# Kernel optimization log

Measured on AMD Instinct MI355X. Metric: run time of the kernel, lower is better.

## Reference

```python
import jax, jax.numpy as jnp
import numpy as np
from jax import lax

B, C, H, W = 4, 64, 256, 256
T, Q = 16, 0.2
C2 = 2 * C


def conv2d(x, w, b, pad):
    y = lax.conv_general_dilated(x, w, (1, 1), [(pad, pad), (pad, pad)],
                                 dimension_numbers=('NCHW', 'OIHW', 'NCHW'))
    return y + b[None, :, None, None]


def setup_inputs() -> dict:
    key = jax.random.key(0)
    ks = jax.random.split(key, 10)
    x = jax.random.normal(ks[0], (B, C, H, W), dtype=jnp.float32)
    lms = jax.random.normal(ks[1], (B, 4, H, W), dtype=jnp.float32)
    # params (kaiming-ish scale)
    W_conv = jax.random.normal(ks[2], (C2, C, 3, 3), dtype=jnp.float32) * (1.0 / np.sqrt(C * 9))
    b_conv = jnp.zeros((C2,), dtype=jnp.float32)
    W_out = jax.random.normal(ks[3], (4, C2), dtype=jnp.float32) * (1.0 / np.sqrt(C2))  # 1x1 conv as matrix
    b_out = jnp.zeros((4,), dtype=jnp.float32)
    W_aue = jax.random.normal(ks[4], (4, C2, 3, 3), dtype=jnp.float32) * (1.0 / np.sqrt(C2 * 9))
    b_aue = jnp.zeros((4,), dtype=jnp.float32)
    # T Bernoulli(1-q) channel masks, fixed for reproducibility  [T, 2C]
    masks = jax.random.bernoulli(ks[5], 1.0 - Q, (T, C2)).astype(jnp.float32)
    return {"x": x, "lms": lms, "W_conv": W_conv, "b_conv": b_conv,
            "W_out": W_out, "b_out": b_out, "W_aue": W_aue, "b_aue": b_aue,
            "masks": masks}


def reference(x, lms, W_conv, b_conv, W_out, b_out, W_aue, b_aue, masks):
    # feature extraction: 3x3 conv C -> 2C
    h = conv2d(x, W_conv, b_conv, 1)                      # [B, 2C, H, W]
    # MC-dropout samples: out(mask_t * h) == (W_out * mask_t) @ h  (1x1 conv is linear)
    Wt = W_out[None, :, :] * masks[:, None, :]            # [T, 4, 2C]
    samples = jnp.tanh(jnp.einsum('toc,bchw->tbohw', Wt, h)
                       + b_out[None, None, :, None, None]) + lms[None]  # [T, B, 4, H, W]
    mean = jnp.mean(samples, axis=0)
    EU = jnp.var(samples, axis=0, ddof=1)                 # unbiased variance over T
    AU = jax.nn.sigmoid(conv2d(h, W_aue, b_aue, 1))       # [B, 4, H, W]
    return (AU, EU, mean)
```

## Files before the change

### kernel.cpp

```cpp
#include <hip/hip_runtime.h>

#define Bsz 4
#define Cin 64
#define C2c 128
#define Hh 256
#define Ww 256
#define Tt 16
#define HW (Hh*Ww)
#define PLANE (Bsz*4*HW)

typedef __attribute__((ext_vector_type(8))) short bf16x8;
typedef __attribute__((ext_vector_type(4))) float f32x4;

#define XT_OFF  0
#define WBF_OFF 33554432
#define WTB_OFF 33701888
#define AUB_OFF 33718272
#define ZP_OFF  33727488

#define N_WTB 8192
#define N_WBF 73728
#define N_AUB 4608
#define N_ZP  64

__device__ __forceinline__ unsigned short f2bf(float f) {
  union { float f; unsigned u; } cv; cv.f = f;
  unsigned u = cv.u;
  unsigned r = (u + 0x7fffu + ((u >> 16) & 1u)) >> 16;
  return (unsigned short)r;
}

__device__ __forceinline__ unsigned cvtpk(float a, float b) {
  unsigned r;
  asm("v_cvt_pk_bf16_f32 %0, %1, %2" : "=v"(r) : "v"(a), "v"(b));
  return r;
}

union U8 { uint2 u2[2]; uint4 u4; bf16x8 v; };

#define GLOAD16(g, l) __builtin_amdgcn_global_load_lds( \
    (const __attribute__((address_space(1))) unsigned int*)(g), \
    (__attribute__((address_space(3))) unsigned int*)(l), 16, 0, 0)

__global__ __launch_bounds__(256) void xtp_kernel(
    const float* __restrict__ x, const float* __restrict__ W_out,
    const float* __restrict__ masks, const float* __restrict__ Wc,
    const float* __restrict__ W_aue,
    unsigned short* __restrict__ xT, unsigned short* __restrict__ Wtb,
    unsigned short* __restrict__ Wbf, unsigned short* __restrict__ Aub,
    unsigned short* __restrict__ Zp) {
  __shared__ unsigned short xs[64 * 132];
  const int tid = threadIdx.x;

  if (blockIdx.z == 4) {
    int i = (blockIdx.y * 2 + blockIdx.x) * 256 + tid;
    if (i < N_WTB) {
      int to = i >> 7, c = i & 127;
      int t = to >> 2, o = to & 3;
      Wtb[i] = f2bf(W_out[o * C2c + c] * masks[t * C2c + c]);
    } else if (i < N_WTB + N_WBF) {
      int idx = i - N_WTB;
      int j = idx & 7;
      int lane = (idx >> 3) & 63;
      int nt = (idx >> 9) & 7;
      int c = idx >> 12;
      int qq = lane >> 4;
      int tap = c >> 1;
      int ic = (c & 1) * 32 + qq * 8 + j;
      int n = nt * 16 + (lane & 15);
      Wbf[idx] = f2bf(Wc[((size_t)n * Cin + ic) * 9 + tap]);
    } else if (i < N_WTB + N_WBF + N_AUB) {
      int idx = i - N_WTB - N_WBF;
      int m = idx / 1152, k = idx % 1152;
      int tap = k >> 7, c = k & 127;
      Aub[idx] = f2bf(W_aue[((size_t)m * C2c + c) * 9 + tap]);
    } else if (i < N_WTB + N_WBF + N_AUB + N_ZP) {
      Zp[i - N_WTB - N_WBF - N_AUB] = 0;
    }
    return;
  }

  const int x0 = blockIdx.x * 128, y = blockIdx.y, bi = blockIdx.z;
  #pragma unroll
  for (int i = 0; i < 8; ++i) {
    int idx = i * 256 + tid;
    int ic = idx >> 5, xq = idx & 31;
    float4 v = *(const float4*)(x + (((size_t)bi * Cin + ic) * Hh + y) * Ww + x0 + xq * 4);
    *(uint2*)(&xs[ic * 132 + xq * 4]) = make_uint2(cvtpk(v.x, v.y), cvtpk(v.z, v.w));
  }
  __syncthreads();
  #pragma unroll
  for (int j = 0; j < 4; ++j) {
    int idx = j * 256 + tid;
    int px = idx >> 3, icg = idx & 7;
    unsigned short u[8];
    #pragma unroll
    for (int k = 0; k < 8; ++k) u[k] = xs[(icg * 8 + k) * 132 + px];
    *(uint4*)(xT + (((size_t)bi * Hh + y) * Ww + (x0 + px)) * Cin + icg * 8) = *(uint4*)u;
  }
}

__global__ __launch_bounds__(256, 3) void fused_kernel(
    const unsigned short* __restrict__ xT, const unsigned short* __restrict__ Wbf,
    const unsigned short* __restrict__ Wtb, const unsigned short* __restrict__ Aub,
    const unsigned short* __restrict__ Zp,
    const float* __restrict__ bc, const float* __restrict__ b_out,
    const float* __restrict__ b_aue, const float* __restrict__ lms,
    float* __restrict__ out) {
  __shared__ __align__(16) unsigned short sh[23040];
  const int tid = threadIdx.x;
  const int x0 = blockIdx.x * 16, y0 = blockIdx.y * 8, bi = blockIdx.z;

  #pragma unroll
  for (int hf = 0; hf < 2; ++hf) {
    #pragma unroll
    for (int i = 0; i < 4; ++i) {
      int g = i * 256 + tid;
      int r = g >> 2;
      int l = (g & 3) ^ (r & 3);
      int pr = r / 20, pc = r - pr * 20;
      int gy = y0 - 2 + pr, gx = x0 - 2 + pc;
      bool ok = (r < 240) && ((unsigned)gy < Hh) && ((unsigned)gx < Ww);
      const unsigned short* src = ok
        ? xT + (((size_t)bi * Hh + gy) * Ww + gx) * Cin + (hf * 4 + l) * 8
        : Zp;
      GLOAD16(src, &sh[hf * 8192 + g * 8]);
    }
  }

  const int lane = tid & 63, wv = tid >> 6;
  const int n16 = lane & 15, q = lane >> 4;

  int rbase[3];
  #pragma unroll
  for (int s = 0; s < 3; ++s) {
    int px = (wv * 3 + s) * 16 + n16;
    int pr = px / 18, pc = px % 18;
    rbase[s] = pr * 20 + pc;
  }

  f32x4 acc[3][8];
  #pragma unroll
  for (int s = 0; s < 3; ++s)
    #pragma unroll
    for (int mt = 0; mt < 8; ++mt) acc[s][mt] = (f32x4){0.f, 0.f, 0.f, 0.f};

  asm volatile("s_waitcnt vmcnt(4)" ::: "memory");
  __builtin_amdgcn_s_barrier();
  __builtin_amdgcn_sched_barrier(0);

  #pragma unroll
  for (int hf = 0; hf < 2; ++hf) {
    if (hf == 1) {
      asm volatile("s_waitcnt vmcnt(0)" ::: "memory");
      __builtin_amdgcn_s_barrier();
      __builtin_amdgcn_sched_barrier(0);
    }
    #pragma unroll
    for (int tap = 0; tap < 9; ++tap) {
      const int dd = (tap / 3) * 20 + (tap % 3);
      const int c = tap * 2 + hf;
      bf16x8 xfr[3];
      #pragma unroll
      for (int s = 0; s < 3; ++s) {
        int rr = rbase[s] + dd;
        int a = hf * 8192 + rr * 32 + ((q ^ (rr & 3)) << 3);
        U8 t; t.u4 = *(const uint4*)(&sh[a]);
        xfr[s] = t.v;
      }
      #pragma unroll
      for (int mh = 0; mh < 2; ++mh) {
        bf16x8 wfr[4];
        const unsigned short* wb = Wbf + ((size_t)(c * 8 + mh * 4) * 64 + lane) * 8;
        #pragma unroll
        for (int i4 = 0; i4 < 4; ++i4)
          wfr[i4] = ((const U8*)(wb + i4 * 512))->v;
        __builtin_amdgcn_s_setprio(1);
        #pragma unroll
        for (int s = 0; s < 3; ++s)
          #pragma unroll
          for (int i4 = 0; i4 < 4; ++i4)
            acc[s][mh * 4 + i4] =
              __builtin_amdgcn_mfma_f32_16x16x32_bf16(wfr[i4], xfr[s], acc[s][mh * 4 + i4], 0, 0, 0);
        __builtin_amdgcn_s_setprio(0);
      }
    }
  }
  __syncthreads();

  #pragma unroll
  for (int s = 0; s < 3; ++s) {
    const int px = (wv * 3 + s) * 16 + n16;
    if (px < 180) {
      const int pr = px / 18, pc = px % 18;
      const int gy = y0 - 1 + pr, gx = x0 - 1 + pc;
      const bool valid = ((unsigned)gy < Hh) && ((unsigned)gx < Ww);
      const int key = px & 15;
      #pragma unroll
      for (int mt = 0; mt < 8; ++mt) {
        const int oc0 = mt * 16 + q * 4;
        const float4 b4 = *(const float4*)(bc + oc0);
        unsigned lo = cvtpk(acc[s][mt][0] + b4.x, acc[s][mt][1] + b4.y);
        unsigned hi = cvtpk(acc[s][mt][2] + b4.z, acc[s][mt][3] + b4.w);
        if (!valid) { lo = 0u; hi = 0u; }
        int a = px * 128 + (((mt * 2 + (q >> 1)) ^ key) << 3) + (q & 1) * 4;
        *(uint2*)(&sh[a]) = make_uint2(lo, hi);
      }
    }
  }
  __syncthreads();

  f32x4 accG[2][4];
  f32x4 accA[2];
  #pragma unroll
  for (int nt = 0; nt < 2; ++nt) {
    accA[nt] = (f32x4){0.f, 0.f, 0.f, 0.f};
    #pragma unroll
    for (int mt = 0; mt < 4; ++mt) accG[nt][mt] = (f32x4){0.f, 0.f, 0.f, 0.f};
  }

  #pragma unroll
  for (int kc = 0; kc < 4; ++kc) {
    bf16x8 afr[4];
    #pragma unroll
    for (int mt = 0; mt < 4; ++mt)
      afr[mt] = ((const U8*)(Wtb + (size_t)(mt * 16 + n16) * C2c + kc * 32 + q * 8))->v;
    #pragma unroll
    for (int nt = 0; nt < 2; ++nt) {
      int hr = (wv * 2 + nt + 1) * 18 + n16 + 1;
      int a = hr * 128 + (((kc * 4 + q) ^ (hr & 15)) << 3);
      U8 b; b.u4 = *(const uint4*)(&sh[a]);
      #pragma unroll
      for (int mt = 0; mt < 4; ++mt)
        accG[nt][mt] = __builtin_amdgcn_mfma_f32_16x16x32_bf16(afr[mt], b.v, accG[nt][mt], 0, 0, 0);
    }
  }

  #pragma unroll
  for (int kc = 0; kc < 36; ++kc) {
    const int tap = kc >> 2, co4 = kc & 3;
    const int dy = tap / 3, dx = tap % 3;
    bf16x8 afr = ((const U8*)(Aub + (size_t)(n16 & 3) * 1152 + kc * 32 + q * 8))->v;
    #pragma unroll
    for (int nt = 0; nt < 2; ++nt) {
      int hr = (wv * 2 + nt + dy) * 18 + n16 + dx;
      int a = hr * 128 + (((co4 * 4 + q) ^ (hr & 15)) << 3);
      U8 b; b.u4 = *(const uint4*)(&sh[a]);
      accA[nt] = __builtin_amdgcn_mfma_f32_16x16x32_bf16(afr, b.v, accA[nt], 0, 0, 0);
    }
  }

  const float b0 = b_out[0], b1 = b_out[1], b2 = b_out[2], b3 = b_out[3];
  const float ba = b_aue[q];
  const int px = x0 + n16;
  #pragma unroll
  for (int nt = 0; nt < 2; ++nt) {
    const int y = y0 + wv * 2 + nt;
    float th[4][4];
    #pragma unroll
    for (int mt = 0; mt < 4; ++mt) {
      #pragma unroll
      for (int r = 0; r < 4; ++r) {
        float bo = (r == 0) ? b0 : (r == 1) ? b1 : (r == 2) ? b2 : b3;
        float v = accG[nt][mt][r] + bo;
        float e = __expf(2.f * v);
        th[mt][r] = 1.f - 2.f / (e + 1.f);
      }
    }
    float mean_r[4], eu_r[4];
    #pragma unroll
    for (int r = 0; r < 4; ++r) {
      float s = th[0][r] + th[1][r] + th[2][r] + th[3][r];
      s += __shfl_xor(s, 16);
      s += __shfl_xor(s, 32);
      float m = s * (1.f / 16.f);
      float d0 = th[0][r] - m, d1 = th[1][r] - m, d2 = th[2][r] - m, d3 = th[3][r] - m;
      float vs = d0 * d0 + d1 * d1 + d2 * d2 + d3 * d3;
      vs += __shfl_xor(vs, 16);
      vs += __shfl_xor(vs, 32);
      mean_r[r] = m;
      eu_r[r] = vs * (1.f / 15.f);
    }
    float au_r[4];
    #pragma unroll
    for (int r = 0; r < 4; ++r) au_r[r] = __shfl(accA[nt][r], n16);

    float m_q  = (q == 0) ? mean_r[0] : (q == 1) ? mean_r[1] : (q == 2) ? mean_r[2] : mean_r[3];
    float eu_q = (q == 0) ? eu_r[0]   : (q == 1) ? eu_r[1]   : (q == 2) ? eu_r[2]   : eu_r[3];
    float au_q = (q == 0) ? au_r[0]   : (q == 1) ? au_r[1]   : (q == 2) ? au_r[2]   : au_r[3];
    au_q = 1.f / (1.f + __expf(-(au_q + ba)));
    size_t oidx = ((size_t)(bi * 4 + q)) * HW + (size_t)y * Ww + px;
    float lm = lms[oidx];
    out[oidx] = au_q;
    out[PLANE + oidx] = eu_q;
    out[2 * (size_t)PLANE + oidx] = m_q + lm;
  }
}

extern "C" void kernel_launch(void* const* d_in, const int* in_sizes, int n_in,
                              void* d_out, int out_size, void* d_ws, size_t ws_size,
                              hipStream_t stream) {
  const float* x      = (const float*)d_in[0];
  const float* lms    = (const float*)d_in[1];
  const float* W_conv = (const float*)d_in[2];
  const float* b_conv = (const float*)d_in[3];
  const float* W_out  = (const float*)d_in[4];
  const float* b_out  = (const float*)d_in[5];
  const float* W_aue  = (const float*)d_in[6];
  const float* b_aue  = (const float*)d_in[7];
  const float* masks  = (const float*)d_in[8];
  float* out = (float*)d_out;

  char* ws = (char*)d_ws;
  unsigned short* xT  = (unsigned short*)(ws + XT_OFF);
  unsigned short* Wbf = (unsigned short*)(ws + WBF_OFF);
  unsigned short* Wtb = (unsigned short*)(ws + WTB_OFF);
  unsigned short* Aub = (unsigned short*)(ws + AUB_OFF);
  unsigned short* Zp  = (unsigned short*)(ws + ZP_OFF);

  xtp_kernel<<<dim3(2, 256, 5), dim3(256), 0, stream>>>(x, W_out, masks, W_conv, W_aue,
                                                        xT, Wtb, Wbf, Aub, Zp);
  fused_kernel<<<dim3(16, 32, 4), dim3(256), 0, stream>>>(xT, Wbf, Wtb, Aub, Zp, b_conv,
                                                          b_out, b_aue, lms, out);
}
```

Baseline: 216.4 us.

## Repartition conv waves by pixel/channel halves and simplify NCHW-to-NHWC transpose

The bf16 transpose kernel drops its LDS staging. Each thread now reads 64 channel values for one pixel with coalesced strided loads and writes a 128-byte NHWC row directly, on a flat 1D grid that also carries the weight-prep blocks. In the fused conv, the four waves are split into two pixel halves times two output-channel halves, each handling 6 pixel tiles by 4 channel tiles. This cuts per-wave weight fragment loads and lets X fragments stream one at a time into MFMAs. The LDS swizzle key changes to (r>>1)&3, presumably to reduce bank conflicts for the new access pattern, at the cost of more x-fragment LDS reads per wave.

```diff
diff --git a/kernel.cpp b/kernel.cpp
--- a/kernel.cpp
+++ b/kernel.cpp
@@ -42,18 +42,17 @@
     (const __attribute__((address_space(1))) unsigned int*)(g), \
     (__attribute__((address_space(3))) unsigned int*)(l), 16, 0, 0)
 
-__global__ __launch_bounds__(256) void xtp_kernel(
+__global__ __launch_bounds__(256) void xt2_kernel(
     const float* __restrict__ x, const float* __restrict__ W_out,
     const float* __restrict__ masks, const float* __restrict__ Wc,
     const float* __restrict__ W_aue,
     unsigned short* __restrict__ xT, unsigned short* __restrict__ Wtb,
     unsigned short* __restrict__ Wbf, unsigned short* __restrict__ Aub,
     unsigned short* __restrict__ Zp) {
-  __shared__ unsigned short xs[64 * 132];
   const int tid = threadIdx.x;
 
-  if (blockIdx.z == 4) {
-    int i = (blockIdx.y * 2 + blockIdx.x) * 256 + tid;
+  if (blockIdx.x >= 1024) {
+    int i = (blockIdx.x - 1024) * 256 + tid;
     if (i < N_WTB) {
       int to = i >> 7, c = i & 127;
       int t = to >> 2, o = to & 3;
@@ -80,23 +79,22 @@
     return;
   }
 
-  const int x0 = blockIdx.x * 128, y = blockIdx.y, bi = blockIdx.z;
-  #pragma unroll
-  for (int i = 0; i < 8; ++i) {
-    int idx = i * 256 + tid;
-    int ic = idx >> 5, xq = idx & 31;
-    float4 v = *(const float4*)(x + (((size_t)bi * Cin + ic) * Hh + y) * Ww + x0 + xq * 4);
-    *(uint2*)(&xs[ic * 132 + xq * 4]) = make_uint2(cvtpk(v.x, v.y), cvtpk(v.z, v.w));
-  }
-  __syncthreads();
-  #pragma unroll
-  for (int j = 0; j < 4; ++j) {
-    int idx = j * 256 + tid;
-    int px = idx >> 3, icg = idx & 7;
-    unsigned short u[8];
-    #pragma unroll
-    for (int k = 0; k < 8; ++k) u[k] = xs[(icg * 8 + k) * 132 + px];
-    *(uint4*)(xT + (((size_t)bi * Hh + y) * Ww + (x0 + px)) * Cin + icg * 8) = *(uint4*)u;
+  int gid = blockIdx.x * 256 + tid;
+  int px = gid & 65535, bi = gid >> 16;
+  const float* xp = x + ((size_t)bi << 22) + px;
+  unsigned short* op = xT + ((size_t)gid << 6);
+  #pragma unroll
+  for (int gp = 0; gp < 4; ++gp) {
+    float v[16];
+    #pragma unroll
+    for (int k = 0; k < 16; ++k) v[k] = xp[((size_t)(gp * 16 + k)) << 16];
+    uint4 a, b;
+    a.x = cvtpk(v[0], v[1]);   a.y = cvtpk(v[2], v[3]);
+    a.z = cvtpk(v[4], v[5]);   a.w = cvtpk(v[6], v[7]);
+    b.x = cvtpk(v[8], v[9]);   b.y = cvtpk(v[10], v[11]);
+    b.z = cvtpk(v[12], v[13]); b.w = cvtpk(v[14], v[15]);
+    *(uint4*)(op + gp * 16) = a;
+    *(uint4*)(op + gp * 16 + 8) = b;
   }
 }
 
@@ -117,7 +115,7 @@
     for (int i = 0; i < 4; ++i) {
       int g = i * 256 + tid;
       int r = g >> 2;
-      int l = (g & 3) ^ (r & 3);
+      int l = (g & 3) ^ ((r >> 1) & 3);
       int pr = r / 20, pc = r - pr * 20;
       int gy = y0 - 2 + pr, gx = x0 - 2 + pc;
       bool ok = (r < 240) && ((unsigned)gy < Hh) && ((unsigned)gx < Ww);
@@ -130,20 +128,21 @@
 
   const int lane = tid & 63, wv = tid >> 6;
   const int n16 = lane & 15, q = lane >> 4;
-
-  int rbase[3];
-  #pragma unroll
-  for (int s = 0; s < 3; ++s) {
-    int px = (wv * 3 + s) * 16 + n16;
+  const int ph = wv >> 1, oh = wv & 1;
+
+  int rbase[6];
+  #pragma unroll
+  for (int s = 0; s < 6; ++s) {
+    int px = ph * 96 + s * 16 + n16;
     int pr = px / 18, pc = px % 18;
     rbase[s] = pr * 20 + pc;
   }
 
-  f32x4 acc[3][8];
-  #pragma unroll
-  for (int s = 0; s < 3; ++s)
-    #pragma unroll
-    for (int mt = 0; mt < 8; ++mt) acc[s][mt] = (f32x4){0.f, 0.f, 0.f, 0.f};
+  f32x4 acc[6][4];
+  #pragma unroll
+  for (int s = 0; s < 6; ++s)
+    #pragma unroll
+    for (int mt = 0; mt < 4; ++mt) acc[s][mt] = (f32x4){0.f, 0.f, 0.f, 0.f};
 
   asm volatile("s_waitcnt vmcnt(4)" ::: "memory");
   __builtin_amdgcn_s_barrier();
@@ -160,50 +159,43 @@
     for (int tap = 0; tap < 9; ++tap) {
       const int dd = (tap / 3) * 20 + (tap % 3);
       const int c = tap * 2 + hf;
-      bf16x8 xfr[3];
-      #pragma unroll
-      for (int s = 0; s < 3; ++s) {
+      bf16x8 wfr[4];
+      const unsigned short* wb = Wbf + ((size_t)(c * 8 + oh * 4) * 64 + lane) * 8;
+      #pragma unroll
+      for (int mt = 0; mt < 4; ++mt)
+        wfr[mt] = ((const U8*)(wb + mt * 512))->v;
+      __builtin_amdgcn_s_setprio(1);
+      #pragma unroll
+      for (int s = 0; s < 6; ++s) {
         int rr = rbase[s] + dd;
-        int a = hf * 8192 + rr * 32 + ((q ^ (rr & 3)) << 3);
+        int a = hf * 8192 + rr * 32 + ((q ^ ((rr >> 1) & 3)) << 3);
         U8 t; t.u4 = *(const uint4*)(&sh[a]);
-        xfr[s] = t.v;
+        #pragma unroll
+        for (int mt = 0; mt < 4; ++mt)
+          acc[s][mt] =
+            __builtin_amdgcn_mfma_f32_16x16x32_bf16(wfr[mt], t.v, acc[s][mt], 0, 0, 0);
       }
-      #pragma unroll
-      for (int mh = 0; mh < 2; ++mh) {
-        bf16x8 wfr[4];
-        const unsigned short* wb = Wbf + ((size_t)(c * 8 + mh * 4) * 64 + lane) * 8;
-        #pragma unroll
-        for (int i4 = 0; i4 < 4; ++i4)
-          wfr[i4] = ((const U8*)(wb + i4 * 512))->v;
-        __builtin_amdgcn_s_setprio(1);
-        #pragma unroll
-        for (int s = 0; s < 3; ++s)
-          #pragma unroll
-          for (int i4 = 0; i4 < 4; ++i4)
-            acc[s][mh * 4 + i4] =
-              __builtin_amdgcn_mfma_f32_16x16x32_bf16(wfr[i4], xfr[s], acc[s][mh * 4 + i4], 0, 0, 0);
-        __builtin_amdgcn_s_setprio(0);
-      }
+      __builtin_amdgcn_s_setprio(0);
     }
   }
   __syncthreads();
 
   #pragma unroll
-  for (int s = 0; s < 3; ++s) {
-    const int px = (wv * 3 + s) * 16 + n16;
+  for (int s = 0; s < 6; ++s) {
+    const int px = ph * 96 + s * 16 + n16;
     if (px < 180) {
       const int pr = px / 18, pc = px % 18;
       const int gy = y0 - 1 + pr, gx = x0 - 1 + pc;
       const bool valid = ((unsigned)gy < Hh) && ((unsigned)gx < Ww);
       const int key = px & 15;
       #pragma unroll
-      for (int mt = 0; mt < 8; ++mt) {
-        const int oc0 = mt * 16 + q * 4;
+      for (int mt = 0; mt < 4; ++mt) {
+        const int oc0 = oh * 64 + mt * 16 + q * 4;
         const float4 b4 = *(const float4*)(bc + oc0);
         unsigned lo = cvtpk(acc[s][mt][0] + b4.x, acc[s][mt][1] + b4.y);
         unsigned hi = cvtpk(acc[s][mt][2] + b4.z, acc[s][mt][3] + b4.w);
         if (!valid) { lo = 0u; hi = 0u; }
-        int a = px * 128 + (((mt * 2 + (q >> 1)) ^ key) << 3) + (q & 1) * 4;
+        int a = px * 128 + (((oc0 >> 3) ^ key) << 3) + (q & 1) * 4;
         *(uint2*)(&sh[a]) = make_uint2(lo, hi);
       }
     }
@@ -318,8 +310,8 @@
   unsigned short* Aub = (unsigned short*)(ws + AUB_OFF);
   unsigned short* Zp  = (unsigned short*)(ws + ZP_OFF);
 
-  xtp_kernel<<<dim3(2, 256, 5), dim3(256), 0, stream>>>(x, W_out, masks, W_conv, W_aue,
-                                                        xT, Wtb, Wbf, Aub, Zp);
+  xt2_kernel<<<dim3(1363), dim3(256), 0, stream>>>(x, W_out, masks, W_conv, W_aue,
+                                                   xT, Wtb, Wbf, Aub, Zp);
   fused_kernel<<<dim3(16, 32, 4), dim3(256), 0, stream>>>(xT, Wbf, Wtb, Aub, Zp, b_conv,
                                                           b_out, b_aue, lms, out);
 }
```

After: 217.4 us. About the same (+0.5%).
